# Optimization experiments

Measured on AMD Instinct MI355X. Metric: run time of the kernel, lower is better.

The kernel has to match this reference:

```python
import jax, jax.numpy as jnp
import numpy as np

HID, INTER, DK = 768, 1536, 128
NEG_INF = 1.0e12
LOG512 = float(np.log(512.0))


def setup_inputs() -> dict:
    key = jax.random.key(0)
    k1, k2, k3 = jax.random.split(key, 3)
    B, S = 4, 2048
    hidden_states = jax.random.normal(k1, (B, S, HID), dtype=jnp.float32)
    attention_mask = jnp.ones((B, S), dtype=jnp.int32)
    # i_dense: hidden -> 2*INTER + DK (no bias); o_dense: INTER -> hidden (no bias)
    Wi = jax.random.normal(k2, (HID, 2 * INTER + DK), dtype=jnp.float32) * (HID ** -0.5)
    Wo = jax.random.normal(k3, (INTER, HID), dtype=jnp.float32) * (INTER ** -0.5)
    q_gamma = jnp.ones((DK,), dtype=jnp.float32)  # ScaleOffset scale, offset=False
    k_gamma = jnp.ones((DK,), dtype=jnp.float32)
    return {"hidden_states": hidden_states, "Wi": Wi, "Wo": Wo,
            "q_gamma": q_gamma, "k_gamma": k_gamma,
            "attention_mask": attention_mask}


def reference(hidden_states, Wi, Wo, q_gamma, k_gamma, attention_mask):
    # i_dense + swish, then split into u, v, qk
    x = jax.nn.silu(jnp.einsum('bsh,ho->bso', hidden_states, Wi))
    u = x[..., :INTER]
    v = x[..., INTER:2 * INTER]
    qk = x[..., 2 * INTER:]
    q = qk * q_gamma
    k = qk * k_gamma
    # single-head attention scores
    a = jnp.einsum('bmd,bnd->bmn', q, k) / (DK ** 0.5)
    mask = attention_mask[:, None, :]  # [B,1,N]
    a = jnp.where(mask == 0, -NEG_INF, a)
    l = jnp.sum(attention_mask, axis=-1, keepdims=True)[:, :, None].astype(a.dtype)  # [B,1,1]
    # softmax_plus: softmax(a * log(l) / log(512))
    A = jax.nn.softmax(a * jnp.log(l) / LOG512, axis=-1)
    # dropout inactive in eval mode
    o = jnp.einsum('bmi,ih->bmh', u * jnp.einsum('bmn,bnd->bmd', A, v), Wo)
    return o
```

## Files before the change

### kernel.cpp

```cpp
#include <hip/hip_runtime.h>
#include <hip/hip_bf16.h>
#include <math.h>

#define BATCH 4
#define SEQ   2048
#define HID   768
#define INTER 1536
#define DK    128
#define NTOT  3200
#define NTOTP 3328
#define MROWS 8192
#define LN512 6.2383246250395075f

typedef _Float16 half8   __attribute__((ext_vector_type(8)));
typedef _Float16 half4   __attribute__((ext_vector_type(4)));
typedef float    floatx4 __attribute__((ext_vector_type(4)));
typedef float    floatx16 __attribute__((ext_vector_type(16)));

typedef const __attribute__((address_space(1))) unsigned int* gas1_t;
typedef __attribute__((address_space(3))) unsigned int* las3_t;

static __device__ __forceinline__ void load16(const _Float16* g, _Float16* l) {
    __builtin_amdgcn_global_load_lds((gas1_t)g, (las3_t)l, 16, 0, 0);
}
#define WAIT_VM(N)    asm volatile("s_waitcnt vmcnt(" #N ")" ::: "memory")
#define WAIT_LGKM0()  asm volatile("s_waitcnt lgkmcnt(0)" ::: "memory")
#define BARRIER_RAW() asm volatile("s_barrier" ::: "memory")
#define GLOAD16(dst, ptr) \
    asm volatile("global_load_dwordx4 %0, %1, off" : "=v"(dst) : "v"(ptr) : "memory")

__global__ __launch_bounds__(256) void prep_kernel(
    const float* __restrict__ H, _Float16* __restrict__ Hb,
    const float* __restrict__ Wi, _Float16* __restrict__ WiT,
    const float* __restrict__ Wo, _Float16* __restrict__ WoT,
    const int* __restrict__ mask, float* __restrict__ scales)
{
    __shared__ _Float16 tile[32][33];
    __shared__ int sh[256];
    const int bid = blockIdx.x, tid = threadIdx.x;
    if (bid < 3072) {
        const int i = (bid * 256 + tid) * 8;
        float4 a = *reinterpret_cast<const float4*>(H + i);
        float4 b = *reinterpret_cast<const float4*>(H + i + 4);
        half8 h = {(_Float16)a.x, (_Float16)a.y, (_Float16)a.z, (_Float16)a.w,
                   (_Float16)b.x, (_Float16)b.y, (_Float16)b.z, (_Float16)b.w};
        *reinterpret_cast<half8*>(Hb + i) = h;
    } else if (bid < 3072 + 2496) {
        const int l = bid - 3072;
        const int c0 = (l % 104) * 32, r0 = (l / 104) * 32;
        const int tx = tid & 31, ty = tid >> 5;
#pragma unroll
        for (int j = 0; j < 32; j += 8)
            tile[tx][ty + j] = (c0 + tx < NTOT)
                ? (_Float16)Wi[(size_t)(r0 + ty + j) * NTOT + c0 + tx]
                : (_Float16)0.0f;
        __syncthreads();
#pragma unroll
        for (int j = 0; j < 32; j += 8)
            WiT[(size_t)(c0 + ty + j) * HID + r0 + tx] = tile[ty + j][tx];
    } else if (bid < 3072 + 2496 + 1152) {
        const int l = bid - (3072 + 2496);
        const int c0 = (l % 24) * 32, r0 = (l / 24) * 32;
        const int tx = tid & 31, ty = tid >> 5;
#pragma unroll
        for (int j = 0; j < 32; j += 8)
            tile[tx][ty + j] = (_Float16)Wo[(size_t)(r0 + ty + j) * HID + c0 + tx];
        __syncthreads();
#pragma unroll
        for (int j = 0; j < 32; j += 8)
            WoT[(size_t)(c0 + ty + j) * INTER + r0 + tx] = tile[ty + j][tx];
    } else {
        const int b = bid - (3072 + 2496 + 1152);
        int s = 0;
        for (int i = tid; i < SEQ; i += 256) s += mask[b * SEQ + i];
        sh[tid] = s;
        __syncthreads();
        for (int off = 128; off > 0; off >>= 1) {
            if (tid < off) sh[tid] += sh[tid + off];
            __syncthreads();
        }
        if (tid == 0) scales[b] = logf((float)sh[0]) / LN512;
    }
}

struct TileCtx {
    int tid, wave, lane, quad, l16, l31, half, wm, wn, c0, c1;
};
static __device__ __forceinline__ TileCtx make_ctx() {
    TileCtx t;
    t.tid = threadIdx.x;
    t.wave = t.tid >> 6; t.lane = t.tid & 63;
    t.quad = t.lane >> 4; t.l16 = t.lane & 15;
    t.l31 = t.lane & 31;  t.half = t.lane >> 5;
    t.wm = (t.wave & 1) * 64;
    t.wn = (t.wave >> 1) * 64;
    t.c0 = t.tid;
    t.c1 = t.tid + 256;
    return t;
}

#define RO32_READ(FR, SLOT) do {                                               \
    const _Float16* Ab_ = smem + (SLOT) * 8192;                                \
    const _Float16* Bb_ = Ab_ + 4096;                                          \
    _Pragma("unroll")                                                          \
    for (int mt = 0; mt < 2; ++mt)                                             \
        _Pragma("unroll")                                                      \
        for (int h = 0; h < 2; ++h)                                            \
            FR##a[mt][h] = *reinterpret_cast<const half8*>(                    \
                Ab_ + (t.wm + mt * 32 + t.l31) * 32 + (((h * 2 + t.half) ^ fsw) * 8)); \
    _Pragma("unroll")                                                          \
    for (int nt = 0; nt < 2; ++nt)                                             \
        _Pragma("unroll")                                                      \
        for (int h = 0; h < 2; ++h)                                            \
            FR##b[nt][h] = *reinterpret_cast<const half8*>(                    \
                Bb_ + (t.wn + nt * 32 + t.l31) * 32 + (((h * 2 + t.half) ^ fsw) * 8)); \
} while (0)

#define RO32_MMA(FR) do {                                                      \
    __builtin_amdgcn_s_setprio(1);                                             \
    _Pragma("unroll")                                                          \
    for (int h = 0; h < 2; ++h)                                                \
        _Pragma("unroll")                                                      \
        for (int mt = 0; mt < 2; ++mt)                                         \
            _Pragma("unroll")                                                  \
            for (int nt = 0; nt < 2; ++nt)                                     \
                acc[mt][nt] = __builtin_amdgcn_mfma_f32_32x32x16_f16(          \
                    FR##a[mt][h], FR##b[nt][h], acc[mt][nt], 0, 0, 0);         \
    __builtin_amdgcn_s_setprio(0);                                             \
} while (0)

#define RO32_STAGE(K) do {                                                     \
    _Float16* ld_ = smem2 + ((K) & 3) * 8192 + t.c0 * 8;                       \
    const int ko_ = (K) << 5;                                                  \
    load16(a0 + ko_, ld_);        load16(a1 + ko_, ld_ + 2048);                \
    load16(b0 + ko_, ld_ + 4096); load16(b1 + ko_, ld_ + 6144);                \
} while (0)

#define RO32_ITER(K, CUR, NXT) do {                                            \
    if ((K) + 2 < nIter) RO32_STAGE((K) + 2);                                  \
    if ((K) + 2 < nIter)      { WAIT_VM(4); }                                  \
    else if ((K) + 1 < nIter) { WAIT_VM(0); }                                  \
    else                      { WAIT_VM(0); }                                  \
    __builtin_amdgcn_sched_barrier(0);                                         \
    BARRIER_RAW();                                                             \
    if ((K) + 1 < nIter) RO32_READ(NXT, ((K) + 1) & 3);                        \
    RO32_MMA(CUR);                                                             \
    WAIT_LGKM0();                                                              \
} while (0)

static __device__ __forceinline__ void gemm_mainloop_ro32(
    const TileCtx& t,
    const _Float16* __restrict__ Ag, int lda,
    const _Float16* __restrict__ Bg, int ldb,
    int K, _Float16* smem, floatx16 acc[2][2])
{
    const int r0i = t.c0 >> 2, s0 = (((r0i >> 1) ^ (r0i >> 3)) & 3);
    const int r1i = t.c1 >> 2, s1 = (((r1i >> 1) ^ (r1i >> 3)) & 3);
    const _Float16* a0 = Ag + (size_t)r0i * lda + ((t.c0 & 3) ^ s0) * 8;
    const _Float16* a1 = Ag + (size_t)r1i * lda + ((t.c1 & 3) ^ s1) * 8;
    const _Float16* b0 = Bg + (size_t)r0i * ldb + ((t.c0 & 3) ^ s0) * 8;
    const _Float16* b1 = Bg + (size_t)r1i * ldb + ((t.c1 & 3) ^ s1) * 8;
    _Float16* smem2 = smem;
    const int nIter = K >> 5;
    const int fsw = ((t.l31 >> 1) ^ (t.l31 >> 3)) & 3;

    half8 pa[2][2], pb[2][2], qa[2][2], qb[2][2];

    RO32_STAGE(0);
    RO32_STAGE(1);
    WAIT_VM(4);
    BARRIER_RAW();
    RO32_READ(p, 0);

    for (int k = 0; k < nIter; k += 2) {
        RO32_ITER(k,     p, q);
        RO32_ITER(k + 1, q, p);
    }
}

__global__ __launch_bounds__(512, 2) void gemm1_kernel(
    const _Float16* __restrict__ Hb, const _Float16* __restrict__ WiT,
    const float* __restrict__ qg, const float* __restrict__ kg,
    _Float16* __restrict__ u, _Float16* __restrict__ vT,
    _Float16* __restrict__ q, _Float16* __restrict__ k)
{
    __shared__ _Float16 smem[65536];
    const int tid = threadIdx.x;
    const int lane = tid & 63, wave = tid >> 6;
    const int quad = lane >> 4, l16 = lane & 15;
    const int wm = wave >> 2, wn = wave & 3;

    const int f = blockIdx.x;
    const int xcd = f & 7, i = f >> 3;
    const int m0 = (xcd * 4 + (i & 3)) * 256;
    const int ntile = i >> 2;
    const int n0 = ntile * 256;

    const _Float16* Ag = Hb  + (size_t)m0 * HID;
    const _Float16* Bg = WiT + (size_t)n0 * HID;

    const int rA = tid >> 2;
    const int csw = ((tid & 3) ^ ((rA >> 1) & 3)) * 8;
    const _Float16* pa0 = Ag + (size_t)rA * HID + csw;
    const _Float16* pa1 = pa0 + (size_t)128 * HID;
    const _Float16* pb0 = Bg + (size_t)rA * HID + csw;
    const _Float16* pb1 = pb0 + (size_t)128 * HID;

    const int sw8 = (l16 >> 1) & 3;
    const int qs  = (quad ^ sw8) * 8;
    const int aoff = (wm * 128 + l16) * 32 + qs;
    const int boff = 8192 + (wn * 64 + l16) * 32 + qs;

    floatx4 acc[8][4] = {};
    half8 pa_[8], pb_[4], qa_[8], qb_[4];

    const int nKt = HID / 32;

#define G1_STAGE(T) do {                                                       \
        _Float16* ld_ = smem + ((T) & 3) * 16384 + tid * 8;                    \
        const int ko_ = (T) << 5;                                              \
        load16(pa0 + ko_, ld_);        load16(pa1 + ko_, ld_ + 4096);          \
        load16(pb0 + ko_, ld_ + 8192); load16(pb1 + ko_, ld_ + 12288);         \
    } while (0)

#define G1_READ(AF, BF, SLOT) do {                                             \
        const _Float16* sl_ = smem + (SLOT) * 16384;                           \
        _Pragma("unroll")                                                      \
        for (int mt = 0; mt < 8; ++mt)                                         \
            AF[mt] = *reinterpret_cast<const half8*>(sl_ + aoff + mt * 512);   \
        _Pragma("unroll")                                                      \
        for (int nt = 0; nt < 4; ++nt)                                         \
            BF[nt] = *reinterpret_cast<const half8*>(sl_ + boff + nt * 512);   \
    } while (0)

#define G1_ITER(T, AFC, BFC, AFN, BFN) do {                                    \
        if ((T) + 3 < nKt) G1_STAGE((T) + 3);                                  \
        if ((T) + 3 < nKt)      { WAIT_VM(8); }                                \
        else if ((T) + 2 < nKt) { WAIT_VM(4); }                                \
        else                    { WAIT_VM(0); }                                \
        __builtin_amdgcn_sched_barrier(0);                                     \
        BARRIER_RAW();                                                         \
        if ((T) + 1 < nKt) G1_READ(AFN, BFN, ((T) + 1) & 3);                   \
        __builtin_amdgcn_s_setprio(1);                                         \
        _Pragma("unroll")                                                      \
        for (int mt = 0; mt < 8; ++mt)                                         \
            _Pragma("unroll")                                                  \
            for (int nt = 0; nt < 4; ++nt)                                     \
                acc[mt][nt] = __builtin_amdgcn_mfma_f32_16x16x32_f16(          \
                    AFC[mt], BFC[nt], acc[mt][nt], 0, 0, 0);                   \
        __builtin_amdgcn_s_setprio(0);                                         \
        WAIT_LGKM0();                                                          \
    } while (0)

    G1_STAGE(0); G1_STAGE(1); G1_STAGE(2);
    WAIT_VM(8);
    BARRIER_RAW();
    G1_READ(pa_, pb_, 0);

    for (int t = 0; t < nKt; t += 2) {
        G1_ITER(t,     pa_, pb_, qa_, qb_);
        G1_ITER(t + 1, qa_, qb_, pa_, pb_);
    }
    __syncthreads();

    if (ntile < 6) {
#pragma unroll
        for (int mt = 0; mt < 8; ++mt) {
#pragma unroll
            for (int nt = 0; nt < 4; ++nt) {
                const int col = n0 + wn * 64 + nt * 16 + l16;
#pragma unroll
                for (int i2 = 0; i2 < 4; ++i2) {
                    const int row = m0 + wm * 128 + mt * 16 + quad * 4 + i2;
                    float x = acc[mt][nt][i2];
                    float y = x / (1.0f + __expf(-x));
                    u[(size_t)row * INTER + col] = (_Float16)y;
                }
            }
        }
    } else if (ntile < 12) {
        const int bb = m0 >> 11, sloc = m0 & (SEQ - 1), cI = n0 - INTER;
#pragma unroll
        for (int mt = 0; mt < 8; ++mt) {
#pragma unroll
            for (int nt = 0; nt < 4; ++nt) {
                const int cl  = wn * 64 + nt * 16 + l16;
                const int rl0 = wm * 128 + mt * 16 + quad * 4;
                half4 pk;
#pragma unroll
                for (int i2 = 0; i2 < 4; ++i2) {
                    float x = acc[mt][nt][i2];
                    pk[i2] = (_Float16)(x / (1.0f + __expf(-x)));
                }
                *reinterpret_cast<half4*>(smem + cl * 256 + (rl0 ^ ((cl & 31) << 3))) = pk;
            }
        }
        __syncthreads();
#pragma unroll
        for (int p = 0; p < 16; ++p) {
            const int chunk = p * 512 + tid;
            const int cl = chunk >> 5, scn = chunk & 31;
            half8 v = *reinterpret_cast<const half8*>(smem + cl * 256 + ((scn ^ (cl & 31)) << 3));
            *reinterpret_cast<half8*>(vT + ((size_t)bb * INTER + cI + cl) * SEQ + sloc + scn * 8) = v;
        }
    } else {
        if (wn < 2) {
#pragma unroll
            for (int mt = 0; mt < 8; ++mt) {
#pragma unroll
                for (int nt = 0; nt < 4; ++nt) {
                    const int cq = wn * 64 + nt * 16 + l16;
                    const float qgv = qg[cq], kgv = kg[cq];
#pragma unroll
                    for (int i2 = 0; i2 < 4; ++i2) {
                        const int row = m0 + wm * 128 + mt * 16 + quad * 4 + i2;
                        float x = acc[mt][nt][i2];
                        float y = x / (1.0f + __expf(-x));
                        q[(size_t)row * DK + cq] = (_Float16)(y * qgv);
                        k[(size_t)row * DK + cq] = (_Float16)(y * kgv);
                    }
                }
            }
        }
    }
}

__global__ __launch_bounds__(256) void scores_kernel(
    const _Float16* __restrict__ q, const _Float16* __restrict__ k,
    const int* __restrict__ mask, const float* __restrict__ scales,
    _Float16* __restrict__ P)
{
    __shared__ _Float16 ps[16 * 2056];
    __shared__ float redmax[4][16];
    __shared__ float redsum[4][16];
    const int f = blockIdx.x;
    const int xcd = f & 7, i = f >> 3;
    const int b = xcd >> 1;
    const int m0 = ((xcd & 1) * 64 + i) * 16;
    const int tid = threadIdx.x;
    const int wave = tid >> 6, lane = tid & 63, quad = lane >> 4, l16 = lane & 15;
    const float scale = scales[b];

    half8 aq[4];
    const _Float16* qrow = q + (b * SEQ + m0 + l16) * DK + quad * 8;
#pragma unroll
    for (int kk = 0; kk < 4; ++kk) aq[kk] = *reinterpret_cast<const half8*>(qrow + kk * 32);

    floatx4 sc[32];
#pragma unroll
    for (int nt = 0; nt < 32; ++nt) {
        int n0 = nt * 64 + wave * 16;
        const _Float16* krow = k + (b * SEQ + n0 + l16) * DK + quad * 8;
        floatx4 acc = {};
#pragma unroll
        for (int kk = 0; kk < 4; ++kk) {
            half8 bq = *reinterpret_cast<const half8*>(krow + kk * 32);
            acc = __builtin_amdgcn_mfma_f32_16x16x32_f16(aq[kk], bq, acc, 0, 0, 0);
        }
        sc[nt] = acc;
    }

    const float rs = 0.08838834764831845f * scale;
    const float mval = -1e12f * scale;
    float rmax[4] = {-3.4e38f, -3.4e38f, -3.4e38f, -3.4e38f};
#pragma unroll
    for (int nt = 0; nt < 32; ++nt) {
        int ncol = nt * 64 + wave * 16 + l16;
        bool mok = mask[b * SEQ + ncol] != 0;
#pragma unroll
        for (int i2 = 0; i2 < 4; ++i2) {
            float s = mok ? sc[nt][i2] * rs : mval;
            sc[nt][i2] = s;
            rmax[i2] = fmaxf(rmax[i2], s);
        }
    }
#pragma unroll
    for (int i2 = 0; i2 < 4; ++i2) {
#pragma unroll
        for (int off = 1; off < 16; off <<= 1)
            rmax[i2] = fmaxf(rmax[i2], __shfl_xor(rmax[i2], off, 64));
    }
    if (l16 == 0) {
#pragma unroll
        for (int i2 = 0; i2 < 4; ++i2) redmax[wave][quad * 4 + i2] = rmax[i2];
    }
    __syncthreads();
#pragma unroll
    for (int i2 = 0; i2 < 4; ++i2) {
        int r = quad * 4 + i2;
        rmax[i2] = fmaxf(fmaxf(redmax[0][r], redmax[1][r]), fmaxf(redmax[2][r], redmax[3][r]));
    }
    float rsum[4] = {0.f, 0.f, 0.f, 0.f};
#pragma unroll
    for (int nt = 0; nt < 32; ++nt) {
#pragma unroll
        for (int i2 = 0; i2 < 4; ++i2) {
            float e = __expf(sc[nt][i2] - rmax[i2]);
            sc[nt][i2] = e;
            rsum[i2] += e;
        }
    }
#pragma unroll
    for (int i2 = 0; i2 < 4; ++i2) {
#pragma unroll
        for (int off = 1; off < 16; off <<= 1) rsum[i2] += __shfl_xor(rsum[i2], off, 64);
    }
    if (l16 == 0) {
#pragma unroll
        for (int i2 = 0; i2 < 4; ++i2) redsum[wave][quad * 4 + i2] = rsum[i2];
    }
    __syncthreads();
#pragma unroll
    for (int i2 = 0; i2 < 4; ++i2) {
        int r = quad * 4 + i2;
        float tot = redsum[0][r] + redsum[1][r] + redsum[2][r] + redsum[3][r];
        float inv = 1.0f / tot;
#pragma unroll
        for (int nt = 0; nt < 32; ++nt) {
            int ncol = nt * 64 + wave * 16 + l16;
            ps[r * 2056 + ncol] = (_Float16)(sc[nt][i2] * inv);
        }
    }
    __syncthreads();
    _Float16* Pfb = P + (size_t)b * SEQ * SEQ;
#pragma unroll
    for (int p = 0; p < 16; ++p) {
        const int chunk = p * 256 + tid;
        const int row = chunk & 15, c8 = chunk >> 4;
        half8 v = *reinterpret_cast<const half8*>(ps + row * 2056 + c8 * 8);
        *reinterpret_cast<half8*>(Pfb + ((size_t)c8 * SEQ + m0 + row) * 8) = v;
    }
}

__global__ __launch_bounds__(256) void pv_kernel(
    const _Float16* __restrict__ Pf, const _Float16* __restrict__ vT,
    _Float16* __restrict__ u)
{
    __shared__ _Float16 smem[16384];
    TileCtx t = make_ctx();
    const int f = blockIdx.x;
    const int xcd = f & 7, i = f >> 3;
    const int b = i / 24, j = i % 24;
    const int m0 = (xcd * 2 + (j & 1)) * 128;
    const int n0 = (j >> 1) * 128;
    const _Float16* Pfb = Pf + (size_t)b * SEQ * SEQ;
    const _Float16* vTb = vT + (size_t)b * INTER * SEQ;

    const int r0i = t.c0 >> 2, s0 = (((r0i >> 1) ^ (r0i >> 3)) & 3);
    const int r1i = t.c1 >> 2, s1 = (((r1i >> 1) ^ (r1i >> 3)) & 3);
    const _Float16* b0 = vTb + (size_t)(n0 + r0i) * SEQ + ((t.c0 & 3) ^ s0) * 8;
    const _Float16* b1 = vTb + (size_t)(n0 + r1i) * SEQ + ((t.c1 & 3) ^ s1) * 8;
    const int fsw = ((t.l31 >> 1) ^ (t.l31 >> 3)) & 3;

    const _Float16* pA0 = Pfb + (size_t)t.half * (SEQ * 8)
                        + (size_t)(m0 + t.wm + t.l31) * 8;
    const _Float16* pA1 = pA0 + 32 * 8;

    floatx16 acc[2][2] = {};
    half8 afA[2][2], afB[2][2], bfA[2][2], bfB[2][2];

#define PV_GLOADA(AF, K) do {                                                  \
        const size_t co_ = (size_t)(K) * 4 * (SEQ * 8);                        \
        GLOAD16(AF[0][0], pA0 + co_);                                          \
        GLOAD16(AF[0][1], pA0 + co_ + 2 * (SEQ * 8));                          \
        GLOAD16(AF[1][0], pA1 + co_);                                          \
        GLOAD16(AF[1][1], pA1 + co_ + 2 * (SEQ * 8));                          \
    } while (0)

#define PV_STAGEB(K) do {                                                      \
        _Float16* ld_ = smem + ((K) & 3) * 4096 + t.c0 * 8;                    \
        const int ko_ = (K) << 5;                                              \
        load16(b0 + ko_, ld_);                                                 \
        load16(b1 + ko_, ld_ + 2048);                                          \
    } while (0)

#define PV_READB(BF, SLOT) do {                                                \
        const _Float16* Bb_ = smem + (SLOT) * 4096;                            \
        _Pragma("unroll")                                                      \
        for (int nt = 0; nt < 2; ++nt)                                         \
            _Pragma("unroll")                                                  \
            for (int h = 0; h < 2; ++h)                                        \
                BF[nt][h] = *reinterpret_cast<const half8*>(                   \
                    Bb_ + (t.wn + nt * 32 + t.l31) * 32 + (((h * 2 + t.half) ^ fsw) * 8)); \
    } while (0)

#define PV_ITER(K, AFC, BFC, AFN, BFN) do {                                    \
        if ((K) + 1 < 64) PV_GLOADA(AFN, (K) + 1);                             \
        if ((K) + 2 < 64) PV_STAGEB((K) + 2);                                  \
        if ((K) + 2 < 64)      { WAIT_VM(6); }                                 \
        else if ((K) + 1 < 64) { WAIT_VM(4); }                                 \
        else                   { WAIT_VM(0); }                                 \
        __builtin_amdgcn_sched_barrier(0);                                     \
        BARRIER_RAW();                                                         \
        if ((K) + 1 < 64) PV_READB(BFN, ((K) + 1) & 3);                        \
        __builtin_amdgcn_s_setprio(1);                                         \
        _Pragma("unroll")                                                      \
        for (int h = 0; h < 2; ++h)                                            \
            _Pragma("unroll")                                                  \
            for (int mt = 0; mt < 2; ++mt)                                     \
                _Pragma("unroll")                                              \
                for (int nt = 0; nt < 2; ++nt)                                 \
                    acc[mt][nt] = __builtin_amdgcn_mfma_f32_32x32x16_f16(      \
                        AFC[mt][h], BFC[nt][h], acc[mt][nt], 0, 0, 0);         \
        __builtin_amdgcn_s_setprio(0);                                         \
        WAIT_LGKM0();                                                          \
    } while (0)

    PV_STAGEB(0);
    PV_STAGEB(1);
    PV_GLOADA(afA, 0);
    WAIT_VM(6);
    BARRIER_RAW();
    PV_READB(bfA, 0);

    for (int k = 0; k < 64; k += 2) {
        PV_ITER(k,     afA, bfA, afB, bfB);
        PV_ITER(k + 1, afB, bfB, afA, bfA);
    }

#pragma unroll
    for (int mt = 0; mt < 2; ++mt) {
#pragma unroll
        for (int nt = 0; nt < 2; ++nt) {
            int col = n0 + t.wn + nt * 32 + t.l31;
#pragma unroll
            for (int reg = 0; reg < 16; ++reg) {
                int row = m0 + t.wm + mt * 32 + (reg & 3) + 8 * (reg >> 2) + 4 * t.half;
                size_t gidx = ((size_t)(b * SEQ + row)) * INTER + col;
                float uv = (float)u[gidx];
                u[gidx] = (_Float16)(acc[mt][nt][reg] * uv);
            }
        }
    }
}

__global__ __launch_bounds__(256) void gemm2_kernel(
    const _Float16* __restrict__ tin, const _Float16* __restrict__ WoT,
    float* __restrict__ out)
{
    __shared__ _Float16 smem[32768];
    TileCtx t = make_ctx();
    const int f = blockIdx.x;
    const int xcd = f & 7, i = f >> 3;
    const int m0 = ((xcd << 3) | (i & 7)) * 128;
    const int n0 = (i >> 3) * 128;

    floatx16 acc[2][2] = {};
    gemm_mainloop_ro32(t, tin + (size_t)m0 * INTER, INTER, WoT + (size_t)n0 * INTER, INTER, INTER, smem, acc);

#pragma unroll
    for (int mt = 0; mt < 2; ++mt) {
#pragma unroll
        for (int nt = 0; nt < 2; ++nt) {
            int col = n0 + t.wn + nt * 32 + t.l31;
#pragma unroll
            for (int reg = 0; reg < 16; ++reg) {
                int row = m0 + t.wm + mt * 32 + (reg & 3) + 8 * (reg >> 2) + 4 * t.half;
                out[(size_t)row * HID + col] = acc[mt][nt][reg];
            }
        }
    }
}

extern "C" void kernel_launch(void* const* d_in, const int* in_sizes, int n_in,
                              void* d_out, int out_size, void* d_ws, size_t ws_size,
                              hipStream_t stream) {
    const float* H    = (const float*)d_in[0];
    const float* Wi   = (const float*)d_in[1];
    const float* Wo   = (const float*)d_in[2];
    const float* qg   = (const float*)d_in[3];
    const float* kg   = (const float*)d_in[4];
    const int*   mask = (const int*)d_in[5];
    float* out = (float*)d_out;

    char* base = (char*)d_ws;
    size_t off = 0;
    auto alloc = [&](size_t bytes) { void* p = base + off; off = (off + bytes + 255) & ~(size_t)255; return p; };
    _Float16* Hb   = (_Float16*)alloc((size_t)MROWS * HID * 2);
    _Float16* WiT  = (_Float16*)alloc((size_t)NTOTP * HID * 2);
    _Float16* WoT  = (_Float16*)alloc((size_t)HID * INTER * 2);
    _Float16* u    = (_Float16*)alloc((size_t)MROWS * INTER * 2);
    _Float16* vT   = (_Float16*)alloc((size_t)BATCH * INTER * SEQ * 2);
    _Float16* q    = (_Float16*)alloc((size_t)MROWS * DK * 2);
    _Float16* k    = (_Float16*)alloc((size_t)MROWS * DK * 2);
    _Float16* P    = (_Float16*)alloc((size_t)BATCH * SEQ * SEQ * 2);
    float*    scales = (float*)alloc(4 * sizeof(float));

    prep_kernel<<<6724, 256, 0, stream>>>(H, Hb, Wi, WiT, Wo, WoT, mask, scales);
    gemm1_kernel<<<416, 512, 0, stream>>>(Hb, WiT, qg, kg, u, vT, q, k);
    scores_kernel<<<512, 256, 0, stream>>>(q, k, mask, scales, P);
    pv_kernel<<<768, 256, 0, stream>>>(P, vT, u);
    gemm2_kernel<<<384, 256, 0, stream>>>(u, WoT, out);
}
```

Baseline: 298.0 us.

## Drop register double-buffering in PV and GEMM2 loops to raise occupancy

Replaces the ping-pong register fragment pipelines in pv_kernel and the gemm2 mainloop with single-buffered fragments, so each iteration reads LDS, waits, then runs the MFMAs. The gemm2 LDS ring shrinks from 4 slots to 3, and both kernels get launch_bounds with a minimum of 3 blocks, aiming for more resident waves and lower register and LDS pressure. The cost is less overlap of LDS reads and global loads with MFMA work inside each wave, plus an extra wait per iteration. The kernels now rely on higher occupancy to hide that latency.

```diff
diff --git a/kernel.cpp b/kernel.cpp
--- a/kernel.cpp
+++ b/kernel.cpp
@@ -99,56 +99,7 @@
     return t;
 }
 
-#define RO32_READ(FR, SLOT) do {                                               \
-    const _Float16* Ab_ = smem + (SLOT) * 8192;                                \
-    const _Float16* Bb_ = Ab_ + 4096;                                          \
-    _Pragma("unroll")                                                          \
-    for (int mt = 0; mt < 2; ++mt)                                             \
-        _Pragma("unroll")                                                      \
-        for (int h = 0; h < 2; ++h)                                            \
-            FR##a[mt][h] = *reinterpret_cast<const half8*>(                    \
-                Ab_ + (t.wm + mt * 32 + t.l31) * 32 + (((h * 2 + t.half) ^ fsw) * 8)); \
-    _Pragma("unroll")                                                          \
-    for (int nt = 0; nt < 2; ++nt)                                             \
-        _Pragma("unroll")                                                      \
-        for (int h = 0; h < 2; ++h)                                            \
-            FR##b[nt][h] = *reinterpret_cast<const half8*>(                    \
-                Bb_ + (t.wn + nt * 32 + t.l31) * 32 + (((h * 2 + t.half) ^ fsw) * 8)); \
-} while (0)
-
-#define RO32_MMA(FR) do {                                                      \
-    __builtin_amdgcn_s_setprio(1);                                             \
-    _Pragma("unroll")                                                          \
-    for (int h = 0; h < 2; ++h)                                                \
-        _Pragma("unroll")                                                      \
-        for (int mt = 0; mt < 2; ++mt)                                         \
-            _Pragma("unroll")                                                  \
-            for (int nt = 0; nt < 2; ++nt)                                     \
-                acc[mt][nt] = __builtin_amdgcn_mfma_f32_32x32x16_f16(          \
-                    FR##a[mt][h], FR##b[nt][h], acc[mt][nt], 0, 0, 0);         \
-    __builtin_amdgcn_s_setprio(0);                                             \
-} while (0)
-
-#define RO32_STAGE(K) do {                                                     \
-    _Float16* ld_ = smem2 + ((K) & 3) * 8192 + t.c0 * 8;                       \
-    const int ko_ = (K) << 5;                                                  \
-    load16(a0 + ko_, ld_);        load16(a1 + ko_, ld_ + 2048);                \
-    load16(b0 + ko_, ld_ + 4096); load16(b1 + ko_, ld_ + 6144);                \
-} while (0)
-
-#define RO32_ITER(K, CUR, NXT) do {                                            \
-    if ((K) + 2 < nIter) RO32_STAGE((K) + 2);                                  \
-    if ((K) + 2 < nIter)      { WAIT_VM(4); }                                  \
-    else if ((K) + 1 < nIter) { WAIT_VM(0); }                                  \
-    else                      { WAIT_VM(0); }                                  \
-    __builtin_amdgcn_sched_barrier(0);                                         \
-    BARRIER_RAW();                                                             \
-    if ((K) + 1 < nIter) RO32_READ(NXT, ((K) + 1) & 3);                        \
-    RO32_MMA(CUR);                                                             \
-    WAIT_LGKM0();                                                              \
-} while (0)
-
-static __device__ __forceinline__ void gemm_mainloop_ro32(
+static __device__ __forceinline__ void gemm_mainloop_lite32(
     const TileCtx& t,
     const _Float16* __restrict__ Ag, int lda,
     const _Float16* __restrict__ Bg, int ldb,
@@ -160,21 +111,52 @@
     const _Float16* a1 = Ag + (size_t)r1i * lda + ((t.c1 & 3) ^ s1) * 8;
     const _Float16* b0 = Bg + (size_t)r0i * ldb + ((t.c0 & 3) ^ s0) * 8;
     const _Float16* b1 = Bg + (size_t)r1i * ldb + ((t.c1 & 3) ^ s1) * 8;
-    _Float16* smem2 = smem;
     const int nIter = K >> 5;
     const int fsw = ((t.l31 >> 1) ^ (t.l31 >> 3)) & 3;
-
-    half8 pa[2][2], pb[2][2], qa[2][2], qb[2][2];
-
-    RO32_STAGE(0);
-    RO32_STAGE(1);
+    half8 af[2][2], bf[2][2];
+
+#define L32_STAGE(KK) do {                                                     \
+        _Float16* ld_ = smem + ((KK) % 3) * 8192 + t.c0 * 8;                   \
+        const int ko_ = (KK) << 5;                                             \
+        load16(a0 + ko_, ld_);        load16(a1 + ko_, ld_ + 2048);            \
+        load16(b0 + ko_, ld_ + 4096); load16(b1 + ko_, ld_ + 6144);            \
+    } while (0)
+
+    L32_STAGE(0);
+    L32_STAGE(1);
     WAIT_VM(4);
     BARRIER_RAW();
-    RO32_READ(p, 0);
-
-    for (int k = 0; k < nIter; k += 2) {
-        RO32_ITER(k,     p, q);
-        RO32_ITER(k + 1, q, p);
+
+    for (int k = 0; k < nIter; ++k) {
+        const _Float16* Ab = smem + (k % 3) * 8192;
+        const _Float16* Bb = Ab + 4096;
+#pragma unroll
+        for (int mt = 0; mt < 2; ++mt)
+#pragma unroll
+            for (int h = 0; h < 2; ++h)
+                af[mt][h] = *reinterpret_cast<const half8*>(
+                    Ab + (t.wm + mt * 32 + t.l31) * 32 + (((h * 2 + t.half) ^ fsw) * 8));
+#pragma unroll
+        for (int nt = 0; nt < 2; ++nt)
+#pragma unroll
+            for (int h = 0; h < 2; ++h)
+                bf[nt][h] = *reinterpret_cast<const half8*>(
+                    Bb + (t.wn + nt * 32 + t.l31) * 32 + (((h * 2 + t.half) ^ fsw) * 8));
+        if (k + 2 < nIter) L32_STAGE(k + 2);
+        if (k + 2 < nIter) { WAIT_VM(4); } else { WAIT_VM(0); }
+        WAIT_LGKM0();
+        __builtin_amdgcn_sched_barrier(0);
+        BARRIER_RAW();
+        __builtin_amdgcn_s_setprio(1);
+#pragma unroll
+        for (int h = 0; h < 2; ++h)
+#pragma unroll
+            for (int mt = 0; mt < 2; ++mt)
+#pragma unroll
+                for (int nt = 0; nt < 2; ++nt)
+                    acc[mt][nt] = __builtin_amdgcn_mfma_f32_32x32x16_f16(
+                        af[mt][h], bf[nt][h], acc[mt][nt], 0, 0, 0);
+        __builtin_amdgcn_s_setprio(0);
     }
 }
 
@@ -432,7 +414,7 @@
     }
 }
 
-__global__ __launch_bounds__(256) void pv_kernel(
+__global__ __launch_bounds__(256, 3) void pv_kernel(
     const _Float16* __restrict__ Pf, const _Float16* __restrict__ vT,
     _Float16* __restrict__ u)
 {
@@ -457,14 +439,14 @@
     const _Float16* pA1 = pA0 + 32 * 8;
 
     floatx16 acc[2][2] = {};
-    half8 afA[2][2], afB[2][2], bfA[2][2], bfB[2][2];
-
-#define PV_GLOADA(AF, K) do {                                                  \
+    half8 af[2][2], bf[2][2];
+
+#define PV_GLOADA(K) do {                                                      \
         const size_t co_ = (size_t)(K) * 4 * (SEQ * 8);                        \
-        GLOAD16(AF[0][0], pA0 + co_);                                          \
-        GLOAD16(AF[0][1], pA0 + co_ + 2 * (SEQ * 8));                          \
-        GLOAD16(AF[1][0], pA1 + co_);                                          \
-        GLOAD16(AF[1][1], pA1 + co_ + 2 * (SEQ * 8));                          \
+        GLOAD16(af[0][0], pA0 + co_);                                          \
+        GLOAD16(af[0][1], pA0 + co_ + 2 * (SEQ * 8));                          \
+        GLOAD16(af[1][0], pA1 + co_);                                          \
+        GLOAD16(af[1][1], pA1 + co_ + 2 * (SEQ * 8));                          \
     } while (0)
 
 #define PV_STAGEB(K) do {                                                      \
@@ -474,48 +456,36 @@
         load16(b1 + ko_, ld_ + 2048);                                          \
     } while (0)
 
-#define PV_READB(BF, SLOT) do {                                                \
-        const _Float16* Bb_ = smem + (SLOT) * 4096;                            \
-        _Pragma("unroll")                                                      \
-        for (int nt = 0; nt < 2; ++nt)                                         \
-            _Pragma("unroll")                                                  \
-            for (int h = 0; h < 2; ++h)                                        \
-                BF[nt][h] = *reinterpret_cast<const half8*>(                   \
-                    Bb_ + (t.wn + nt * 32 + t.l31) * 32 + (((h * 2 + t.half) ^ fsw) * 8)); \
-    } while (0)
-
-#define PV_ITER(K, AFC, BFC, AFN, BFN) do {                                    \
-        if ((K) + 1 < 64) PV_GLOADA(AFN, (K) + 1);                             \
-        if ((K) + 2 < 64) PV_STAGEB((K) + 2);                                  \
-        if ((K) + 2 < 64)      { WAIT_VM(6); }                                 \
-        else if ((K) + 1 < 64) { WAIT_VM(4); }                                 \
-        else                   { WAIT_VM(0); }                                 \
-        __builtin_amdgcn_sched_barrier(0);                                     \
-        BARRIER_RAW();                                                         \
-        if ((K) + 1 < 64) PV_READB(BFN, ((K) + 1) & 3);                        \
-        __builtin_amdgcn_s_setprio(1);                                         \
-        _Pragma("unroll")                                                      \
-        for (int h = 0; h < 2; ++h)                                            \
-            _Pragma("unroll")                                                  \
-            for (int mt = 0; mt < 2; ++mt)                                     \
-                _Pragma("unroll")                                              \
-                for (int nt = 0; nt < 2; ++nt)                                 \
-                    acc[mt][nt] = __builtin_amdgcn_mfma_f32_32x32x16_f16(      \
-                        AFC[mt][h], BFC[nt][h], acc[mt][nt], 0, 0, 0);         \
-        __builtin_amdgcn_s_setprio(0);                                         \
-        WAIT_LGKM0();                                                          \
-    } while (0)
-
     PV_STAGEB(0);
     PV_STAGEB(1);
-    PV_GLOADA(afA, 0);
-    WAIT_VM(6);
+    PV_GLOADA(0);
+    WAIT_VM(4);
     BARRIER_RAW();
-    PV_READB(bfA, 0);
-
-    for (int k = 0; k < 64; k += 2) {
-        PV_ITER(k,     afA, bfA, afB, bfB);
-        PV_ITER(k + 1, afB, bfB, afA, bfA);
+
+    for (int k = 0; k < 64; ++k) {
+        const _Float16* Bb = smem + (k & 3) * 4096;
+#pragma unroll
+        for (int nt = 0; nt < 2; ++nt)
+#pragma unroll
+            for (int h = 0; h < 2; ++h)
+                bf[nt][h] = *reinterpret_cast<const half8*>(
+                    Bb + (t.wn + nt * 32 + t.l31) * 32 + (((h * 2 + t.half) ^ fsw) * 8));
+        if (k + 2 < 64) PV_STAGEB(k + 2);
+        if (k <= 61) { WAIT_VM(2); } else { WAIT_VM(0); }
+        WAIT_LGKM0();
+        __builtin_amdgcn_sched_barrier(0);
+        BARRIER_RAW();
+        __builtin_amdgcn_s_setprio(1);
+#pragma unroll
+        for (int h = 0; h < 2; ++h)
+#pragma unroll
+            for (int mt = 0; mt < 2; ++mt)
+#pragma unroll
+                for (int nt = 0; nt < 2; ++nt)
+                    acc[mt][nt] = __builtin_amdgcn_mfma_f32_32x32x16_f16(
+                        af[mt][h], bf[nt][h], acc[mt][nt], 0, 0, 0);
+        __builtin_amdgcn_s_setprio(0);
+        if (k + 1 < 64) PV_GLOADA(k + 1);
     }
 
 #pragma unroll
@@ -534,11 +504,11 @@
     }
 }
 
-__global__ __launch_bounds__(256) void gemm2_kernel(
+__global__ __launch_bounds__(256, 3) void gemm2_kernel(
     const _Float16* __restrict__ tin, const _Float16* __restrict__ WoT,
     float* __restrict__ out)
 {
-    __shared__ _Float16 smem[32768];
+    __shared__ _Float16 smem[24576];
     TileCtx t = make_ctx();
     const int f = blockIdx.x;
     const int xcd = f & 7, i = f >> 3;
@@ -546,7 +516,7 @@
     const int n0 = (i >> 3) * 128;
 
     floatx16 acc[2][2] = {};
-    gemm_mainloop_ro32(t, tin + (size_t)m0 * INTER, INTER, WoT + (size_t)n0 * INTER, INTER, INTER, smem, acc);
+    gemm_mainloop_lite32(t, tin + (size_t)m0 * INTER, INTER, WoT + (size_t)n0 * INTER, INTER, INTER, smem, acc);
 
 #pragma unroll
     for (int mt = 0; mt < 2; ++mt) {
```

Result: no change. 296.9 us (-0.4%).

## Replace gemm2 4-slot register-prefetch pipeline with 3-stage LDS ring mainloop

Applied to the files above, without the earlier changes.

Rewrites the gemm2 K-loop from a 4-slot LDS ring with register double-buffered fragments (reading the next tile's fragments during the current MFMAs) to a 3-slot LDS ring that loads fragments and runs the MFMAs within the same iteration. Shared memory for gemm2 shrinks from 64KB to 48KB, which may allow more resident blocks per CU. In exchange, the LDS-read latency is no longer hidden behind the previous iteration's MFMAs, and the setprio hints are dropped.

```diff
diff --git a/kernel.cpp b/kernel.cpp
--- a/kernel.cpp
+++ b/kernel.cpp
@@ -99,56 +99,7 @@
     return t;
 }
 
-#define RO32_READ(FR, SLOT) do {                                               \
-    const _Float16* Ab_ = smem + (SLOT) * 8192;                                \
-    const _Float16* Bb_ = Ab_ + 4096;                                          \
-    _Pragma("unroll")                                                          \
-    for (int mt = 0; mt < 2; ++mt)                                             \
-        _Pragma("unroll")                                                      \
-        for (int h = 0; h < 2; ++h)                                            \
-            FR##a[mt][h] = *reinterpret_cast<const half8*>(                    \
-                Ab_ + (t.wm + mt * 32 + t.l31) * 32 + (((h * 2 + t.half) ^ fsw) * 8)); \
-    _Pragma("unroll")                                                          \
-    for (int nt = 0; nt < 2; ++nt)                                             \
-        _Pragma("unroll")                                                      \
-        for (int h = 0; h < 2; ++h)                                            \
-            FR##b[nt][h] = *reinterpret_cast<const half8*>(                    \
-                Bb_ + (t.wn + nt * 32 + t.l31) * 32 + (((h * 2 + t.half) ^ fsw) * 8)); \
-} while (0)
-
-#define RO32_MMA(FR) do {                                                      \
-    __builtin_amdgcn_s_setprio(1);                                             \
-    _Pragma("unroll")                                                          \
-    for (int h = 0; h < 2; ++h)                                                \
-        _Pragma("unroll")                                                      \
-        for (int mt = 0; mt < 2; ++mt)                                         \
-            _Pragma("unroll")                                                  \
-            for (int nt = 0; nt < 2; ++nt)                                     \
-                acc[mt][nt] = __builtin_amdgcn_mfma_f32_32x32x16_f16(          \
-                    FR##a[mt][h], FR##b[nt][h], acc[mt][nt], 0, 0, 0);         \
-    __builtin_amdgcn_s_setprio(0);                                             \
-} while (0)
-
-#define RO32_STAGE(K) do {                                                     \
-    _Float16* ld_ = smem2 + ((K) & 3) * 8192 + t.c0 * 8;                       \
-    const int ko_ = (K) << 5;                                                  \
-    load16(a0 + ko_, ld_);        load16(a1 + ko_, ld_ + 2048);                \
-    load16(b0 + ko_, ld_ + 4096); load16(b1 + ko_, ld_ + 6144);                \
-} while (0)
-
-#define RO32_ITER(K, CUR, NXT) do {                                            \
-    if ((K) + 2 < nIter) RO32_STAGE((K) + 2);                                  \
-    if ((K) + 2 < nIter)      { WAIT_VM(4); }                                  \
-    else if ((K) + 1 < nIter) { WAIT_VM(0); }                                  \
-    else                      { WAIT_VM(0); }                                  \
-    __builtin_amdgcn_sched_barrier(0);                                         \
-    BARRIER_RAW();                                                             \
-    if ((K) + 1 < nIter) RO32_READ(NXT, ((K) + 1) & 3);                        \
-    RO32_MMA(CUR);                                                             \
-    WAIT_LGKM0();                                                              \
-} while (0)
-
-static __device__ __forceinline__ void gemm_mainloop_ro32(
+static __device__ __forceinline__ void gemm_mainloop_3s32(
     const TileCtx& t,
     const _Float16* __restrict__ Ag, int lda,
     const _Float16* __restrict__ Bg, int ldb,
@@ -156,25 +107,60 @@
 {
     const int r0i = t.c0 >> 2, s0 = (((r0i >> 1) ^ (r0i >> 3)) & 3);
     const int r1i = t.c1 >> 2, s1 = (((r1i >> 1) ^ (r1i >> 3)) & 3);
-    const _Float16* a0 = Ag + (size_t)r0i * lda + ((t.c0 & 3) ^ s0) * 8;
-    const _Float16* a1 = Ag + (size_t)r1i * lda + ((t.c1 & 3) ^ s1) * 8;
-    const _Float16* b0 = Bg + (size_t)r0i * ldb + ((t.c0 & 3) ^ s0) * 8;
-    const _Float16* b1 = Bg + (size_t)r1i * ldb + ((t.c1 & 3) ^ s1) * 8;
-    _Float16* smem2 = smem;
+    const int ak0 = ((t.c0 & 3) ^ s0) * 8;
+    const int ak1 = ((t.c1 & 3) ^ s1) * 8;
+    const _Float16* a0 = Ag + (size_t)r0i * lda + ak0;
+    const _Float16* a1 = Ag + (size_t)r1i * lda + ak1;
+    const _Float16* b0 = Bg + (size_t)r0i * ldb + ak0;
+    const _Float16* b1 = Bg + (size_t)r1i * ldb + ak1;
+    _Float16* Asl = smem + t.c0 * 8;
+    _Float16* Bsl = smem + 12288 + t.c0 * 8;
     const int nIter = K >> 5;
+
     const int fsw = ((t.l31 >> 1) ^ (t.l31 >> 3)) & 3;
 
-    half8 pa[2][2], pb[2][2], qa[2][2], qb[2][2];
-
-    RO32_STAGE(0);
-    RO32_STAGE(1);
-    WAIT_VM(4);
-    BARRIER_RAW();
-    RO32_READ(p, 0);
-
-    for (int k = 0; k < nIter; k += 2) {
-        RO32_ITER(k,     p, q);
-        RO32_ITER(k + 1, q, p);
+    load16(a0, Asl);        load16(a1, Asl + 2048);
+    load16(b0, Bsl);        load16(b1, Bsl + 2048);
+    if (nIter > 1) {
+        load16(a0 + 32, Asl + 4096); load16(a1 + 32, Asl + 6144);
+        load16(b0 + 32, Bsl + 4096); load16(b1 + 32, Bsl + 6144);
+    }
+
+    int sc = 0, sp = 2;
+    for (int k = 0; k < nIter; ++k) {
+        if (k + 1 < nIter) { WAIT_VM(4); } else { WAIT_VM(0); }
+        BARRIER_RAW();
+        if (k + 2 < nIter) {
+            const int off = sp * 4096;
+            const int k0 = (k + 2) << 5;
+            load16(a0 + k0, Asl + off); load16(a1 + k0, Asl + off + 2048);
+            load16(b0 + k0, Bsl + off); load16(b1 + k0, Bsl + off + 2048);
+        }
+        const _Float16* Ab = smem + sc * 4096;
+        const _Float16* Bb = smem + 12288 + sc * 4096;
+        half8 af[2][2], bf[2][2];
+#pragma unroll
+        for (int mt = 0; mt < 2; ++mt)
+#pragma unroll
+            for (int h = 0; h < 2; ++h)
+                af[mt][h] = *reinterpret_cast<const half8*>(
+                    Ab + (t.wm + mt * 32 + t.l31) * 32 + (((h * 2 + t.half) ^ fsw) * 8));
+#pragma unroll
+        for (int nt = 0; nt < 2; ++nt)
+#pragma unroll
+            for (int h = 0; h < 2; ++h)
+                bf[nt][h] = *reinterpret_cast<const half8*>(
+                    Bb + (t.wn + nt * 32 + t.l31) * 32 + (((h * 2 + t.half) ^ fsw) * 8));
+#pragma unroll
+        for (int h = 0; h < 2; ++h)
+#pragma unroll
+            for (int mt = 0; mt < 2; ++mt)
+#pragma unroll
+                for (int nt = 0; nt < 2; ++nt)
+                    acc[mt][nt] = __builtin_amdgcn_mfma_f32_32x32x16_f16(af[mt][h], bf[nt][h], acc[mt][nt], 0, 0, 0);
+        WAIT_LGKM0();
+        sc = (sc == 2) ? 0 : sc + 1;
+        sp = (sp == 2) ? 0 : sp + 1;
     }
 }
 
@@ -538,7 +524,7 @@
     const _Float16* __restrict__ tin, const _Float16* __restrict__ WoT,
     float* __restrict__ out)
 {
-    __shared__ _Float16 smem[32768];
+    __shared__ _Float16 smem[24576];
     TileCtx t = make_ctx();
     const int f = blockIdx.x;
     const int xcd = f & 7, i = f >> 3;
@@ -546,7 +532,7 @@
     const int n0 = (i >> 3) * 128;
 
     floatx16 acc[2][2] = {};
-    gemm_mainloop_ro32(t, tin + (size_t)m0 * INTER, INTER, WoT + (size_t)n0 * INTER, INTER, INTER, smem, acc);
+    gemm_mainloop_3s32(t, tin + (size_t)m0 * INTER, INTER, WoT + (size_t)n0 * INTER, INTER, INTER, smem, acc);
 
 #pragma unroll
     for (int mt = 0; mt < 2; ++mt) {
```

Result: slower. 313.3 us (+5.1%).
